# Optimization experiments

Hardware: AMD Instinct MI355X
Metric: run time of the kernel (lower is better)

## Reference

```python
import jax, jax.numpy as jnp
import numpy as np

NUM_HEADS = 8

def _ln(x, w, b, eps=1e-5):
    m = x.mean(-1, keepdims=True)
    v = ((x - m) ** 2).mean(-1, keepdims=True)
    return (x - m) / jnp.sqrt(v + eps) * w + b

def _conv3(x, w, b):
    y = jax.lax.conv_general_dilated(x, w, (1, 1), 'SAME',
                                     dimension_numbers=('NCHW', 'OIHW', 'NCHW'))
    return y + b[None, :, None, None]

def _pos_encoding(c, h, w, dtype):
    # first c//2 channels: x position in [0,1]; next c//2: y position
    px = jnp.broadcast_to(jnp.linspace(0, 1, w, dtype=dtype)[None, :], (h, w))
    py = jnp.broadcast_to(jnp.linspace(0, 1, h, dtype=dtype)[:, None], (h, w))
    pe = jnp.concatenate([jnp.broadcast_to(px, (c // 2, h, w)),
                          jnp.broadcast_to(py, (c // 2, h, w))], axis=0)
    return pe[None]  # [1,c,h,w]

def _pixel_shuffle(x, r=2):
    b, c4, h, w = x.shape
    c = c4 // (r * r)
    return x.reshape(b, c, r, r, h, w).transpose(0, 1, 4, 2, 5, 3).reshape(b, c, h * r, w * r)

def _forward(x, text_hidden, proj_w, proj_b, cf_w, cf_b,
             blk_qw, blk_qb, blk_kw, blk_kb, blk_vw, blk_vb,
             blk_ow, blk_ob, blk_ln1w, blk_ln1b, blk_ln2w, blk_ln2b,
             up_w, up_b, cl_w, cl_b):
    B = x.shape[0]
    # text projection: [B, L, text_dim] -> [B, L, C]
    tf = jnp.einsum('bld,cd->blc', text_hidden, proj_w) + proj_b
    feat = _conv3(x, cf_w, cf_b)  # [B, C, H, W]
    _, C, H, W = feat.shape
    L = tf.shape[1]
    hd = C // NUM_HEADS
    scale = hd ** (-0.5)
    pe = _pos_encoding(C, H, W, feat.dtype)

    def block(feat, p):
        qw, qb, kw, kb, vw, vb, ow, ob, l1w, l1b, l2w, l2b = p
        q = jnp.einsum('oi,bihw->bohw', qw, feat) + qb[None, :, None, None]
        q = q + pe * 0.05
        q_flat = q.reshape(B, C, H * W).transpose(0, 2, 1)  # [B, HW, C]
        q_norm = _ln(q_flat, l1w, l1b)
        qh = q_norm.reshape(B, H * W, NUM_HEADS, hd).transpose(0, 2, 1, 3)
        k = jnp.einsum('blc,oc->blo', tf, kw) + kb
        v = jnp.einsum('blc,oc->blo', tf, vw) + vb
        kn = _ln(k, l2w, l2b)
        kh = kn.reshape(B, L, NUM_HEADS, hd).transpose(0, 2, 1, 3)
        vh = v.reshape(B, L, NUM_HEADS, hd).transpose(0, 2, 1, 3)
        attn = jax.nn.softmax(jnp.einsum('bhnd,bhld->bhnl', qh, kh) * scale, axis=-1)
        out = jnp.einsum('bhnl,bhld->bhnd', attn, vh)          # [B, H8, HW, hd]
        out = out.transpose(0, 2, 1, 3).reshape(B, H * W, C)   # [B, HW, C]
        out = out.transpose(0, 2, 1).reshape(B, C, H, W)
        out = jnp.einsum('oi,bihw->bohw', ow, out) + ob[None, :, None, None]
        return out + feat, None

    blk_params = (blk_qw, blk_qb, blk_kw, blk_kb, blk_vw, blk_vb,
                  blk_ow, blk_ob, blk_ln1w, blk_ln1b, blk_ln2w, blk_ln2b)
    feat, _ = jax.lax.scan(block, feat, blk_params)

    for i in range(up_w.shape[0]):
        feat = jax.nn.relu(_pixel_shuffle(_conv3(feat, up_w[i], up_b[i]), 2))
    return _conv3(feat, cl_w, cl_b)


def setup_inputs() -> dict:
    key = jax.random.key(0)
    ks = jax.random.split(key, 20)
    B, H, W = 8, 64, 64
    C, D, L, NB = 64, 512, 77, 16
    s = 0.05
    inp = {
        'x': jax.random.normal(ks[0], (B, 3, H, W), jnp.float32),
        'text_hidden': jax.random.normal(ks[1], (B, L, D), jnp.float32),
        'proj_w': jax.random.normal(ks[2], (C, D), jnp.float32) * 0.01,
        'proj_b': jnp.zeros((C,), jnp.float32),
        'cf_w': jax.random.normal(ks[3], (C, 3, 3, 3), jnp.float32) * s,
        'cf_b': jnp.zeros((C,), jnp.float32),
        'blk_qw': jax.random.normal(ks[4], (NB, C, C), jnp.float32) * s,
        'blk_qb': jnp.zeros((NB, C), jnp.float32),
        'blk_kw': jax.random.normal(ks[5], (NB, C, C), jnp.float32) * 0.01,
        'blk_kb': jnp.zeros((NB, C), jnp.float32),
        'blk_vw': jax.random.normal(ks[6], (NB, C, C), jnp.float32) * 0.01,
        'blk_vb': jnp.zeros((NB, C), jnp.float32),
        'blk_ow': jax.random.normal(ks[7], (NB, C, C), jnp.float32) * s,
        'blk_ob': jnp.zeros((NB, C), jnp.float32),
        'blk_ln1w': jnp.ones((NB, C), jnp.float32),
        'blk_ln1b': jnp.zeros((NB, C), jnp.float32),
        'blk_ln2w': jnp.ones((NB, C), jnp.float32),
        'blk_ln2b': jnp.zeros((NB, C), jnp.float32),
        'up_w': jax.random.normal(ks[8], (2, C * 4, C, 3, 3), jnp.float32) * s,
        'up_b': jnp.zeros((2, C * 4), jnp.float32),
        'cl_w': jax.random.normal(ks[9], (3, C, 3, 3), jnp.float32) * s,
        'cl_b': jnp.zeros((3,), jnp.float32),
    }
    return inp


def reference(x, text_hidden, proj_w, proj_b, cf_w, cf_b,
              blk_qw, blk_qb, blk_kw, blk_kb, blk_vw, blk_vb,
              blk_ow, blk_ob, blk_ln1w, blk_ln1b, blk_ln2w, blk_ln2b,
              up_w, up_b, cl_w, cl_b):
    return _forward(x, text_hidden, proj_w, proj_b, cf_w, cf_b,
                    blk_qw, blk_qb, blk_kw, blk_kb, blk_vw, blk_vb,
                    blk_ow, blk_ob, blk_ln1w, blk_ln1b, blk_ln2w, blk_ln2b,
                    up_w, up_b, cl_w, cl_b)
```

## Files before the change

### kernel.cpp

```cpp
#include <hip/hip_runtime.h>
#include <math.h>

#define BATCH 8
#define C 64
#define NH 8
#define HD 8
#define LTXT 77
#define H0 64
#define W0 64
#define HW0 (H0*W0)

typedef __attribute__((ext_vector_type(8))) short bfrag;
typedef __attribute__((ext_vector_type(4))) float ffrag;
typedef __attribute__((ext_vector_type(8))) unsigned short us8;
typedef __attribute__((ext_vector_type(4))) unsigned short us4;
typedef __attribute__((ext_vector_type(2))) float f2;

#if defined(__has_builtin)
#if __has_builtin(__builtin_amdgcn_exp2f)
#define EXP2(x) __builtin_amdgcn_exp2f(x)
#else
#define EXP2(x) exp2f(x)
#endif
#else
#define EXP2(x) exp2f(x)
#endif

__device__ __forceinline__ unsigned short f2bf(float f) {
    unsigned u = __builtin_bit_cast(unsigned, f);
    u += 0x7fff + ((u >> 16) & 1);
    return (unsigned short)(u >> 16);
}

__global__ void text_proj_kernel(const float* __restrict__ th, const float* __restrict__ pw,
                                 const float* __restrict__ pb, float* __restrict__ tf) {
    __shared__ float sh[512];
    int bl = blockIdx.x;
    int c = threadIdx.x;
    const float* row = th + (size_t)bl * 512;
    for (int i = c; i < 512; i += 64) sh[i] = row[i];
    __syncthreads();
    const float* wrow = pw + c * 512;
    float acc = pb[c];
    for (int i = 0; i < 512; i += 4) {
        acc += sh[i] * wrow[i] + sh[i+1] * wrow[i+1] + sh[i+2] * wrow[i+2] + sh[i+3] * wrow[i+3];
    }
    tf[bl * 64 + c] = acc;
}

__global__ void __launch_bounds__(256)
prep_kernel(const float* __restrict__ x, const float* __restrict__ cf_w,
            const float* __restrict__ cf_b, float* __restrict__ feat,
            const float* __restrict__ up_w,
            unsigned short* __restrict__ PW1, unsigned short* __restrict__ PW2,
            const float* __restrict__ cl_w, unsigned short* __restrict__ PWF,
            const float* __restrict__ qw, const float* __restrict__ ow,
            unsigned short* __restrict__ PQ, unsigned short* __restrict__ PO) {
    int blk = blockIdx.x;
    if (blk < 8192) {
        int idx = blk * 256 + threadIdx.x;
        int wx = idx & 63;
        int h = (idx >> 6) & 63;
        int o = (idx >> 12) & 63;
        int b = idx >> 18;
        const float* wr = cf_w + o * 27;
        float acc = cf_b[o];
        for (int ci = 0; ci < 3; ci++) {
            for (int ky = 0; ky < 3; ky++) {
                int y = h + ky - 1;
                if ((unsigned)y >= 64u) continue;
                const float* xr = x + (((size_t)b * 3 + ci) * 64 + y) * 64;
                const float* wk = wr + ci * 9 + ky * 3;
                if (wx > 0) acc += xr[wx - 1] * wk[0];
                acc += xr[wx] * wk[1];
                if (wx < 63) acc += xr[wx + 1] * wk[2];
            }
        }
        feat[idx] = acc;
    } else if (blk < 8192 + 1152) {
        int e0 = blk - 8192;
        int st = e0 / 576;
        int e = (e0 % 576) * 256 + threadIdx.x;
        const float* w = up_w + (size_t)st * 147456;
        unsigned short* d = st ? PW2 : PW1;
        int j = e & 7, n = (e >> 3) & 255, q = (e >> 11) & 3, s = (e >> 13) & 1, t = e >> 14;
        int c = n & 63, g = n >> 6;
        int co = 4 * c + g, ci = 32 * s + 8 * q + j;
        d[e] = f2bf(w[co * 576 + ci * 9 + t]);
    } else if (blk < 8192 + 1152 + 36) {
        int e = (blk - 8192 - 1152) * 256 + threadIdx.x;
        int j = e & 7, n = (e >> 3) & 15, q = (e >> 7) & 3, s = (e >> 9) & 1, t = e >> 10;
        int ci = 32 * s + 8 * q + j;
        float v = (n < 3) ? cl_w[n * 576 + ci * 9 + t] : 0.f;
        PWF[e] = f2bf(v);
    } else {
        int e = (blk - 8192 - 1152 - 36) * 256 + threadIdx.x;
        int j = e & 7, n = (e >> 3) & 63, quad = (e >> 9) & 3, kt = (e >> 11) & 1, layer = e >> 12;
        int c = kt * 32 + quad * 8 + j;
        PQ[e] = f2bf(qw[layer * 4096 + n * 64 + c]);
        PO[e] = f2bf(ow[layer * 4096 + n * 64 + c]);
    }
}

__global__ void kv_all_kernel(const float* __restrict__ tf,
                              const float* __restrict__ kw, const float* __restrict__ kb,
                              const float* __restrict__ vw, const float* __restrict__ vb,
                              const float* __restrict__ l2w, const float* __restrict__ l2b,
                              float* __restrict__ kvbuf) {
    __shared__ float sh[64];
    int g = blockIdx.x;
    int bl = g % (BATCH * LTXT);
    int blk = g / (BATCH * LTXT);
    int o = threadIdx.x;
    sh[o] = tf[bl * 64 + o];
    __syncthreads();
    const float* kr = kw + blk * 4096 + o * 64;
    const float* vr = vw + blk * 4096 + o * 64;
    float ka = kb[blk * 64 + o], va = vb[blk * 64 + o];
    for (int c2 = 0; c2 < 64; c2++) {
        float t = sh[c2];
        ka += t * kr[c2];
        va += t * vr[c2];
    }
    float s = ka;
    for (int off = 32; off; off >>= 1) s += __shfl_xor(s, off, 64);
    float mean = s * (1.0f / 64.0f);
    float d = ka - mean;
    float s2 = d * d;
    for (int off = 32; off; off >>= 1) s2 += __shfl_xor(s2, off, 64);
    float rstd = rsqrtf(s2 * (1.0f / 64.0f) + 1e-5f);
    float kn = (d * rstd * l2w[blk * 64 + o] + l2b[blk * 64 + o]) * 0.51006973f;
    size_t base = ((size_t)blk * (BATCH * LTXT) + bl) * 128;
    int hd = o >> 3, ch = o & 7;
    kvbuf[base + hd * 16 + ch]     = kn;
    kvbuf[base + hd * 16 + 8 + ch] = va;
}

__global__ void __launch_bounds__(1024, 8)
attn_all_kernel(const float* __restrict__ feat,
                const float* __restrict__ kvbuf,
                const unsigned short* __restrict__ PQ, const unsigned short* __restrict__ PO,
                const float* __restrict__ qb_a, const float* __restrict__ ob_a,
                const float* __restrict__ l1w_a, const float* __restrict__ l1b_a,
                unsigned short* __restrict__ X1) {
    __shared__ __attribute__((aligned(16))) unsigned short sfb[64][72];
    __shared__ __attribute__((aligned(16))) unsigned short sob[64][72];
    __shared__ __attribute__((aligned(16))) float qf[64][68];
    __shared__ float so[64][64];
    __shared__ __attribute__((aligned(16))) float red[2][4][64];
    __shared__ float ss1[8][64];

    int b = blockIdx.x >> 6;
    int tile = blockIdx.x & 63;
    int n0 = tile << 6;
    int wv = __builtin_amdgcn_readfirstlane(threadIdx.x >> 6);
    int lane = threadIdx.x & 63;
    int p = lane;
    int quad = lane >> 4, n16 = lane & 15;
    int mt = wv >> 2, nt = wv & 3;
    int o0 = wv * 4;
    int h = wv >> 1, half = wv & 1;
    int a0 = h * 8;
    const float* fbase = feat + ((size_t)b << 18) + n0;

    float rres[4];
#pragma unroll
    for (int j = 0; j < 4; j++) rres[j] = fbase[(o0 + j) * HW0 + p];
    {
        us4 v;
#pragma unroll
        for (int j = 0; j < 4; j++) v[j] = f2bf(rres[j]);
        *(us4*)&sfb[p][o0] = v;
    }

    const float pxk = 0.05f / 63.0f;
    float py005 = (float)tile * pxk;
    __syncthreads();

#pragma unroll 1
    for (int layer = 0; layer < 16; layer++) {
        const float* qb = qb_a + layer * 64;
        const float* ob = ob_a + layer * 64;
        const float* l1w = l1w_a + layer * 64;
        const float* l1b = l1b_a + layer * 64;

        {
            bfrag af0 = *(const bfrag*)&sfb[mt * 16 + n16][quad * 8];
            bfrag af1 = *(const bfrag*)&sfb[mt * 16 + n16][32 + quad * 8];
            const unsigned short* bq = PQ + layer * 4096 + (size_t)((quad * 64) + nt * 16 + n16) * 8;
            bfrag bf0 = *(const bfrag*)bq;
            bfrag bf1 = *(const bfrag*)(bq + 2048);
            ffrag cc = (ffrag)0.f;
            cc = __builtin_amdgcn_mfma_f32_16x16x32_bf16(af0, bf0, cc, 0, 0, 0);
            cc = __builtin_amdgcn_mfma_f32_16x16x32_bf16(af1, bf1, cc, 0, 0, 0);
            int cch = nt * 16 + n16;
            float qbv = qb[cch];
            int p0 = mt * 16 + quad * 4;
            float pe0 = (nt < 2) ? (float)p0 * pxk : py005;
            float ped = (nt < 2) ? pxk : 0.f;
            float ov[4];
            ov[0] = cc[0] + qbv + pe0;
            ov[1] = cc[1] + qbv + pe0 + ped;
            ov[2] = cc[2] + qbv + pe0 + 2.f * ped;
            ov[3] = cc[3] + qbv + pe0 + 3.f * ped;
            float4 o4 = {ov[0], ov[1], ov[2], ov[3]};
            *(float4*)&qf[cch][p0] = o4;

            float sv[4], sq[4];
#pragma unroll
            for (int r = 0; r < 4; r++) {
                float s = ov[r], s2v = ov[r] * ov[r];
                s += __shfl_xor(s, 1);  s2v += __shfl_xor(s2v, 1);
                s += __shfl_xor(s, 2);  s2v += __shfl_xor(s2v, 2);
                s += __shfl_xor(s, 4);  s2v += __shfl_xor(s2v, 4);
                s += __shfl_xor(s, 8);  s2v += __shfl_xor(s2v, 8);
                sv[r] = s; sq[r] = s2v;
            }
            if (n16 == 0) {
                *(float4*)&red[0][nt][p0] = (float4){sv[0], sv[1], sv[2], sv[3]};
                *(float4*)&red[1][nt][p0] = (float4){sq[0], sq[1], sq[2], sq[3]};
            }
        }
        __syncthreads();

        {
            float ts = red[0][0][p] + red[0][1][p] + red[0][2][p] + red[0][3][p];
            float ts2 = red[1][0][p] + red[1][1][p] + red[1][2][p] + red[1][3][p];
            float mean = ts * (1.0f / 64.0f);
            float var = ts2 * (1.0f / 64.0f) - mean * mean;
            float rstd = rsqrtf(var + 1e-5f);

            f2 qv[4];
#pragma unroll
            for (int j = 0; j < 4; j++) {
                float qa  = (qf[a0 + 2 * j][p]     - mean) * rstd * l1w[a0 + 2 * j]     + l1b[a0 + 2 * j];
                float qbv = (qf[a0 + 2 * j + 1][p] - mean) * rstd * l1w[a0 + 2 * j + 1] + l1b[a0 + 2 * j + 1];
                qv[j][0] = qa;
                qv[j][1] = qbv;
            }
            const float* kvb = kvbuf + ((size_t)layer * BATCH * LTXT + (size_t)b * LTXT) * 128 + h * 16;
            int l0 = half ? 39 : 0;
            int l1 = half ? 77 : 39;
            float ssum = 0.f;
            f2 acc2[4] = {(f2)0.f, (f2)0.f, (f2)0.f, (f2)0.f};
            int l = l0;
            for (; l + 3 <= l1; l += 3) {
                const float4* ra = (const float4*)(kvb + (size_t)l * 128);
                const float4* rb = (const float4*)(kvb + (size_t)(l + 1) * 128);
                const float4* rc = (const float4*)(kvb + (size_t)(l + 2) * 128);
                float4 ka0 = ra[0], ka1 = ra[1], va0 = ra[2], va1 = ra[3];
                float4 kb0 = rb[0], kb1 = rb[1], vb0 = rb[2], vb1 = rb[3];
                float4 kc0 = rc[0], kc1 = rc[1], vc0 = rc[2], vc1 = rc[3];

                f2 da = qv[0] * (f2){ka0.x, ka0.y};
                da += qv[1] * (f2){ka0.z, ka0.w};
                da += qv[2] * (f2){ka1.x, ka1.y};
                da += qv[3] * (f2){ka1.z, ka1.w};
                float ea = EXP2(da[0] + da[1]);
                ssum += ea;
                f2 ea2 = {ea, ea};
                acc2[0] += ea2 * (f2){va0.x, va0.y};
                acc2[1] += ea2 * (f2){va0.z, va0.w};
                acc2[2] += ea2 * (f2){va1.x, va1.y};
                acc2[3] += ea2 * (f2){va1.z, va1.w};

                f2 db = qv[0] * (f2){kb0.x, kb0.y};
                db += qv[1] * (f2){kb0.z, kb0.w};
                db += qv[2] * (f2){kb1.x, kb1.y};
                db += qv[3] * (f2){kb1.z, kb1.w};
                float eb = EXP2(db[0] + db[1]);
                ssum += eb;
                f2 eb2 = {eb, eb};
                acc2[0] += eb2 * (f2){vb0.x, vb0.y};
                acc2[1] += eb2 * (f2){vb0.z, vb0.w};
                acc2[2] += eb2 * (f2){vb1.x, vb1.y};
                acc2[3] += eb2 * (f2){vb1.z, vb1.w};

                f2 dc = qv[0] * (f2){kc0.x, kc0.y};
                dc += qv[1] * (f2){kc0.z, kc0.w};
                dc += qv[2] * (f2){kc1.x, kc1.y};
                dc += qv[3] * (f2){kc1.z, kc1.w};
                float ec = EXP2(dc[0] + dc[1]);
                ssum += ec;
                f2 ec2 = {ec, ec};
                acc2[0] += ec2 * (f2){vc0.x, vc0.y};
                acc2[1] += ec2 * (f2){vc0.z, vc0.w};
                acc2[2] += ec2 * (f2){vc1.x, vc1.y};
                acc2[3] += ec2 * (f2){vc1.z, vc1.w};
            }
            for (; l < l1; l++) {
                const float4* r = (const float4*)(kvb + (size_t)l * 128);
                float4 k0 = r[0], k1 = r[1], v0 = r[2], v1 = r[3];
                f2 d2 = qv[0] * (f2){k0.x, k0.y};
                d2 += qv[1] * (f2){k0.z, k0.w};
                d2 += qv[2] * (f2){k1.x, k1.y};
                d2 += qv[3] * (f2){k1.z, k1.w};
                float e = EXP2(d2[0] + d2[1]);
                ssum += e;
                f2 e2 = {e, e};
                acc2[0] += e2 * (f2){v0.x, v0.y};
                acc2[1] += e2 * (f2){v0.z, v0.w};
                acc2[2] += e2 * (f2){v1.x, v1.y};
                acc2[3] += e2 * (f2){v1.z, v1.w};
            }
            if (half) {
#pragma unroll
                for (int j = 0; j < 4; j++) {
                    so[a0 + 2 * j][p] = acc2[j][0];
                    so[a0 + 2 * j + 1][p] = acc2[j][1];
                }
                ss1[h][p] = ssum;
            }
            __syncthreads();
            if (!half) {
                float inv = 1.0f / (ssum + ss1[h][p]);
                us8 v;
#pragma unroll
                for (int j = 0; j < 4; j++) {
                    v[2*j]   = f2bf((acc2[j][0] + so[a0 + 2*j][p]) * inv);
                    v[2*j+1] = f2bf((acc2[j][1] + so[a0 + 2*j+1][p]) * inv);
                }
                *(us8*)&sob[p][a0] = v;
            }
        }
        __syncthreads();

        {
            bfrag af0 = *(const bfrag*)&sob[mt * 16 + n16][quad * 8];
            bfrag af1 = *(const bfrag*)&sob[mt * 16 + n16][32 + quad * 8];
            const unsigned short* bo = PO + layer * 4096 + (size_t)((quad * 64) + nt * 16 + n16) * 8;
            bfrag bf0 = *(const bfrag*)bo;
            bfrag bf1 = *(const bfrag*)(bo + 2048);
            ffrag cc = (ffrag)0.f;
            cc = __builtin_amdgcn_mfma_f32_16x16x32_bf16(af0, bf0, cc, 0, 0, 0);
            cc = __builtin_amdgcn_mfma_f32_16x16x32_bf16(af1, bf1, cc, 0, 0, 0);
            int cch = nt * 16 + n16;
            float obv = ob[cch];
            int p0 = mt * 16 + quad * 4;
            float4 o4;
            o4.x = cc[0] + obv; o4.y = cc[1] + obv; o4.z = cc[2] + obv; o4.w = cc[3] + obv;
            *(float4*)&qf[cch][p0] = o4;
        }
        __syncthreads();

        {
            us4 v;
#pragma unroll
            for (int j = 0; j < 4; j++) {
                rres[j] += qf[o0 + j][p];
                v[j] = f2bf(rres[j]);
            }
            *(us4*)&sfb[p][o0] = v;
        }
        __syncthreads();
    }

    us4 v;
#pragma unroll
    for (int j = 0; j < 4; j++) v[j] = f2bf(rres[j]);
    *(us4*)(X1 + ((size_t)(b * 4096 + n0 + p)) * 64 + o0) = v;
}

__global__ void __launch_bounds__(512)
upconv_mfma_kernel(const unsigned short* __restrict__ X, const unsigned short* __restrict__ Bp,
                   const float* __restrict__ bias, unsigned short* __restrict__ Y,
                   int Hin, int Win) {
    __shared__ __attribute__((aligned(16))) unsigned short sx[3 * 66 * 72];

    int wv = threadIdx.x >> 6;
    int lane = threadIdx.x & 63;
    int q = lane >> 4, n16 = lane & 15;
    int m0 = blockIdx.x * 64;
    int hw = Hin * Win;
    int b = m0 / hw, rem = m0 % hw;
    int h = rem / Win, w0 = rem % Win;
    const unsigned short* Xb = X + (size_t)b * hw * 64;

    const us8 z8 = (us8)(unsigned short)0;
    for (int e = threadIdx.x; e < 1584; e += 512) {
        int ch8 = e & 7;
        int pxi = (e >> 3) % 66;
        int row = e / 528;
        int hh = h + row - 1, wp = w0 + pxi - 1;
        us8 v = z8;
        if ((unsigned)hh < (unsigned)Hin && (unsigned)wp < (unsigned)Win)
            v = *(const us8*)(Xb + ((size_t)hh * Win + wp) * 64 + ch8 * 8);
        *(us8*)&sx[row * 4752 + pxi * 72 + ch8 * 8] = v;
    }
    __syncthreads();

    ffrag acc[4][2];
#pragma unroll
    for (int i = 0; i < 4; i++)
#pragma unroll
        for (int j2 = 0; j2 < 2; j2++) acc[i][j2] = (ffrag)0.f;

    int npb = wv * 32;

    for (int t = 0; t < 9; t++) {
        int dy = t / 3, dx = t % 3;
        bfrag af[4][2];
#pragma unroll
        for (int mt = 0; mt < 4; mt++) {
            const unsigned short* sp = &sx[dy * 4752 + (mt * 16 + n16 + dx) * 72 + q * 8];
            af[mt][0] = *(const bfrag*)sp;
            af[mt][1] = *(const bfrag*)(sp + 32);
        }
#pragma unroll
        for (int s = 0; s < 2; s++) {
#pragma unroll
            for (int nt = 0; nt < 2; nt++) {
                bfrag bf = *(const bfrag*)(Bp + (size_t)((((t * 2 + s) * 4 + q) * 256) + npb + nt * 16 + n16) * 8);
#pragma unroll
                for (int mt = 0; mt < 4; mt++)
                    acc[mt][nt] = __builtin_amdgcn_mfma_f32_16x16x32_bf16(af[mt][s], bf, acc[mt][nt], 0, 0, 0);
            }
        }
    }

    int g = wv >> 1;
    int r1 = wv >> 2, r2 = (wv >> 1) & 1;
    int cbase = (wv & 1) * 32;
    float bv[2];
#pragma unroll
    for (int nt = 0; nt < 2; nt++) bv[nt] = bias[4 * (cbase + nt * 16 + n16) + g];
    int Wo = Win * 2;
    unsigned short* Yb = Y + ((size_t)b * Hin * 2 * Wo + (size_t)(2 * h + r1) * Wo + r2) * 64;
#pragma unroll
    for (int mt = 0; mt < 4; mt++) {
#pragma unroll
        for (int r = 0; r < 4; r++) {
            int m = mt * 16 + q * 4 + r;
            unsigned short* dst = Yb + (size_t)(2 * (w0 + m)) * 64;
#pragma unroll
            for (int nt = 0; nt < 2; nt++) {
                float v = acc[mt][nt][r] + bv[nt];
                v = fmaxf(v, 0.f);
                dst[cbase + nt * 16 + n16] = f2bf(v);
            }
        }
    }
}

__global__ void __launch_bounds__(256)
final_mfma_kernel(const unsigned short* __restrict__ X, const unsigned short* __restrict__ Bp,
                  const float* __restrict__ bias, float* __restrict__ out) {
    __shared__ __attribute__((aligned(16))) unsigned short sx[6 * 66 * 72];

    int t0 = blockIdx.x;
    int wseg = t0 & 3;
    int rg = (t0 >> 2) & 63;
    int b = t0 >> 8;
    int y0 = rg * 4, w0 = wseg * 64;
    int wv = threadIdx.x >> 6, lane = threadIdx.x & 63;
    int q = lane >> 4, n16 = lane & 15;
    const unsigned short* Xb = X + (size_t)b * 65536 * 64;

    const us8 z8 = (us8)(unsigned short)0;
    for (int e = threadIdx.x; e < 3168; e += 256) {
        int ch8 = e & 7;
        int pxi = (e >> 3) % 66;
        int row = e / 528;
        int hh = y0 - 1 + row, wp = w0 - 1 + pxi;
        us8 v = z8;
        if ((unsigned)hh < 256u && (unsigned)wp < 256u)
            v = *(const us8*)(Xb + ((size_t)hh * 256 + wp) * 64 + ch8 * 8);
        *(us8*)&sx[row * 4752 + pxi * 72 + ch8 * 8] = v;
    }
    __syncthreads();

    ffrag acc[4];
#pragma unroll
    for (int i = 0; i < 4; i++) acc[i] = (ffrag)0.f;

    for (int t = 0; t < 9; t++) {
        int dy = t / 3, dx = t % 3;
        bfrag af[4][2];
#pragma unroll
        for (int mt = 0; mt < 4; mt++) {
            const unsigned short* sp = &sx[(wv + dy) * 4752 + (mt * 16 + n16 + dx) * 72 + q * 8];
            af[mt][0] = *(const bfrag*)sp;
            af[mt][1] = *(const bfrag*)(sp + 32);
        }
#pragma unroll
        for (int s = 0; s < 2; s++) {
            bfrag bf = *(const bfrag*)(Bp + (size_t)((((t * 2 + s) * 4 + q) * 16) + n16) * 8);
#pragma unroll
            for (int mt = 0; mt < 4; mt++)
                acc[mt] = __builtin_amdgcn_mfma_f32_16x16x32_bf16(af[mt][s], bf, acc[mt], 0, 0, 0);
        }
    }

    if (n16 < 3) {
        float bj = bias[n16];
        float* ob = out + (((size_t)b * 3 + n16) * 256 + (y0 + wv)) * 256;
#pragma unroll
        for (int mt = 0; mt < 4; mt++)
#pragma unroll
            for (int r = 0; r < 4; r++)
                ob[w0 + mt * 16 + q * 4 + r] = acc[mt][r] + bj;
    }
}

extern "C" void kernel_launch(void* const* d_in, const int* in_sizes, int n_in,
                              void* d_out, int out_size, void* d_ws, size_t ws_size,
                              hipStream_t stream) {
    const float* x      = (const float*)d_in[0];
    const float* th     = (const float*)d_in[1];
    const float* proj_w = (const float*)d_in[2];
    const float* proj_b = (const float*)d_in[3];
    const float* cf_w   = (const float*)d_in[4];
    const float* cf_b   = (const float*)d_in[5];
    const float* qw     = (const float*)d_in[6];
    const float* qb     = (const float*)d_in[7];
    const float* kw     = (const float*)d_in[8];
    const float* kb     = (const float*)d_in[9];
    const float* vw     = (const float*)d_in[10];
    const float* vb     = (const float*)d_in[11];
    const float* ow     = (const float*)d_in[12];
    const float* ob     = (const float*)d_in[13];
    const float* l1w    = (const float*)d_in[14];
    const float* l1b    = (const float*)d_in[15];
    const float* l2w    = (const float*)d_in[16];
    const float* l2b    = (const float*)d_in[17];
    const float* up_w   = (const float*)d_in[18];
    const float* up_b   = (const float*)d_in[19];
    const float* cl_w   = (const float*)d_in[20];
    const float* cl_b   = (const float*)d_in[21];

    float* ws   = (float*)d_ws;
    float* feat = ws;
    float* tf   = feat + 2097152;
    float* kvbuf = tf + 39424;
    unsigned short* X1  = (unsigned short*)(kvbuf + 1261568);
    unsigned short* X2  = X1 + 2097152;
    unsigned short* X3  = X2 + 8388608;
    unsigned short* PW1 = X3 + 33554432;
    unsigned short* PW2 = PW1 + 147456;
    unsigned short* PWF = PW2 + 147456;
    unsigned short* PQ  = PWF + 9216;
    unsigned short* PO  = PQ + 65536;

    hipLaunchKernelGGL(prep_kernel, dim3(8192 + 1152 + 36 + 256), dim3(256), 0, stream,
                       x, cf_w, cf_b, feat, up_w, PW1, PW2, cl_w, PWF, qw, ow, PQ, PO);
    hipLaunchKernelGGL(text_proj_kernel, dim3(BATCH * LTXT), dim3(64), 0, stream,
                       th, proj_w, proj_b, tf);
    hipLaunchKernelGGL(kv_all_kernel, dim3(16 * BATCH * LTXT), dim3(64), 0, stream,
                       tf, kw, kb, vw, vb, l2w, l2b, kvbuf);

    hipLaunchKernelGGL(attn_all_kernel, dim3(BATCH * (HW0 / 64)), dim3(1024), 0, stream,
                       feat, kvbuf, PQ, PO, qb, ob, l1w, l1b, X1);

    hipLaunchKernelGGL(upconv_mfma_kernel, dim3(BATCH * 64 * 64 / 64), dim3(512), 0, stream,
                       X1, PW1, up_b, X2, 64, 64);
    hipLaunchKernelGGL(upconv_mfma_kernel, dim3(BATCH * 128 * 128 / 64), dim3(512), 0, stream,
                       X2, PW2, up_b + 256, X3, 128, 128);
    hipLaunchKernelGGL(final_mfma_kernel, dim3(BATCH * 64 * 4), dim3(256), 0, stream,
                       X3, PWF, cl_b, (float*)d_out);
}
```

Baseline: 488.1 us.

## Process two input rows per block in upconv kernel to reuse halo and weights

```diff
diff --git a/kernel.cpp b/kernel.cpp
--- a/kernel.cpp
+++ b/kernel.cpp
@@ -365,23 +365,25 @@
 upconv_mfma_kernel(const unsigned short* __restrict__ X, const unsigned short* __restrict__ Bp,
                    const float* __restrict__ bias, unsigned short* __restrict__ Y,
                    int Hin, int Win) {
-    __shared__ __attribute__((aligned(16))) unsigned short sx[3 * 66 * 72];
+    __shared__ __attribute__((aligned(16))) unsigned short sx[4 * 66 * 72];
 
     int wv = threadIdx.x >> 6;
     int lane = threadIdx.x & 63;
     int q = lane >> 4, n16 = lane & 15;
-    int m0 = blockIdx.x * 64;
-    int hw = Hin * Win;
-    int b = m0 / hw, rem = m0 % hw;
-    int h = rem / Win, w0 = rem % Win;
-    const unsigned short* Xb = X + (size_t)b * hw * 64;
+    int tiles_w = Win >> 6;
+    int t0 = blockIdx.x;
+    int wseg = t0 % tiles_w;
+    int h2 = (t0 / tiles_w) % (Hin >> 1);
+    int b = t0 / (tiles_w * (Hin >> 1));
+    int h0 = h2 * 2, w0 = wseg * 64;
+    const unsigned short* Xb = X + (size_t)b * Hin * Win * 64;
 
     const us8 z8 = (us8)(unsigned short)0;
-    for (int e = threadIdx.x; e < 1584; e += 512) {
+    for (int e = threadIdx.x; e < 2112; e += 512) {
         int ch8 = e & 7;
         int pxi = (e >> 3) % 66;
         int row = e / 528;
-        int hh = h + row - 1, wp = w0 + pxi - 1;
+        int hh = h0 + row - 1, wp = w0 + pxi - 1;
         us8 v = z8;
         if ((unsigned)hh < (unsigned)Hin && (unsigned)wp < (unsigned)Win)
             v = *(const us8*)(Xb + ((size_t)hh * Win + wp) * 64 + ch8 * 8);
@@ -389,27 +391,29 @@
     }
     __syncthreads();
 
-    ffrag acc[4][2];
+    ffrag acc[4][4];
 #pragma unroll
     for (int i = 0; i < 4; i++)
 #pragma unroll
-        for (int j2 = 0; j2 < 2; j2++) acc[i][j2] = (ffrag)0.f;
-
-    int npb = wv * 32;
+        for (int j2 = 0; j2 < 4; j2++) acc[i][j2] = (ffrag)0.f;
+
+    int ri = wv >> 2;
+    int g = wv & 3;
+    int npb = g * 64;
 
     for (int t = 0; t < 9; t++) {
         int dy = t / 3, dx = t % 3;
         bfrag af[4][2];
 #pragma unroll
         for (int mt = 0; mt < 4; mt++) {
-            const unsigned short* sp = &sx[dy * 4752 + (mt * 16 + n16 + dx) * 72 + q * 8];
+            const unsigned short* sp = &sx[(ri + dy) * 4752 + (mt * 16 + n16 + dx) * 72 + q * 8];
             af[mt][0] = *(const bfrag*)sp;
             af[mt][1] = *(const bfrag*)(sp + 32);
         }
 #pragma unroll
         for (int s = 0; s < 2; s++) {
 #pragma unroll
-            for (int nt = 0; nt < 2; nt++) {
+            for (int nt = 0; nt < 4; nt++) {
                 bfrag bf = *(const bfrag*)(Bp + (size_t)((((t * 2 + s) * 4 + q) * 256) + npb + nt * 16 + n16) * 8);
 #pragma unroll
                 for (int mt = 0; mt < 4; mt++)
@@ -418,14 +422,12 @@
         }
     }
 
-    int g = wv >> 1;
-    int r1 = wv >> 2, r2 = (wv >> 1) & 1;
-    int cbase = (wv & 1) * 32;
-    float bv[2];
-#pragma unroll
-    for (int nt = 0; nt < 2; nt++) bv[nt] = bias[4 * (cbase + nt * 16 + n16) + g];
+    int r1 = g >> 1, r2 = g & 1;
+    float bv[4];
+#pragma unroll
+    for (int nt = 0; nt < 4; nt++) bv[nt] = bias[4 * (nt * 16 + n16) + g];
     int Wo = Win * 2;
-    unsigned short* Yb = Y + ((size_t)b * Hin * 2 * Wo + (size_t)(2 * h + r1) * Wo + r2) * 64;
+    unsigned short* Yb = Y + ((size_t)b * Hin * 2 * Wo + (size_t)(2 * (h0 + ri) + r1) * Wo + r2) * 64;
 #pragma unroll
     for (int mt = 0; mt < 4; mt++) {
 #pragma unroll
@@ -433,10 +435,10 @@
             int m = mt * 16 + q * 4 + r;
             unsigned short* dst = Yb + (size_t)(2 * (w0 + m)) * 64;
 #pragma unroll
-            for (int nt = 0; nt < 2; nt++) {
+            for (int nt = 0; nt < 4; nt++) {
                 float v = acc[mt][nt][r] + bv[nt];
                 v = fmaxf(v, 0.f);
-                dst[cbase + nt * 16 + n16] = f2bf(v);
+                dst[nt * 16 + n16] = f2bf(v);
             }
         }
     }
@@ -551,9 +553,9 @@
     hipLaunchKernelGGL(attn_all_kernel, dim3(BATCH * (HW0 / 64)), dim3(1024), 0, stream,
                        feat, kvbuf, PQ, PO, qb, ob, l1w, l1b, X1);
 
-    hipLaunchKernelGGL(upconv_mfma_kernel, dim3(BATCH * 64 * 64 / 64), dim3(512), 0, stream,
+    hipLaunchKernelGGL(upconv_mfma_kernel, dim3(BATCH * 32 * 1), dim3(512), 0, stream,
                        X1, PW1, up_b, X2, 64, 64);
-    hipLaunchKernelGGL(upconv_mfma_kernel, dim3(BATCH * 128 * 128 / 64), dim3(512), 0, stream,
+    hipLaunchKernelGGL(upconv_mfma_kernel, dim3(BATCH * 64 * 2), dim3(512), 0, stream,
                        X2, PW2, up_b + 256, X3, 128, 128);
     hipLaunchKernelGGL(final_mfma_kernel, dim3(BATCH * 64 * 4), dim3(256), 0, stream,
                        X3, PWF, cl_b, (float*)d_out);
```

Result: no change. 487.4 us (-0.2%).
